# Kernel optimization log

Measured on AMD Instinct MI355X. Metric: run time of the kernel, lower is better.

## Reference

```python
import jax, jax.numpy as jnp
import numpy as np

K = 0.5   # k constant from init
QS = 0.1  # qs constant from init


def setup_inputs() -> dict:
    key = jax.random.key(0)
    k1, k2, k3 = jax.random.split(key, 3)
    B, OUT, M, IN = 512, 128, 8, 512
    x = jax.random.normal(k1, (B, IN), dtype=jnp.float32)
    W = jax.random.uniform(k2, (OUT, M, IN), dtype=jnp.float32)
    q = jax.random.uniform(k3, (OUT, M, IN), dtype=jnp.float32)
    return {"x": x, "W": W, "q": q}


def reference(x, W, q):
    # x: [B, IN]; W, q: [OUT, M, IN]
    # dendritic: relu(k * (x*W - q)), summed over input dim
    syn = jax.nn.relu(K * (x[:, None, None, :] * W - q))  # [B, OUT, M, IN]
    dend = jax.nn.relu(jnp.sum(syn, axis=3))              # [B, OUT, M]
    soma = jnp.sum(dend, axis=2)                          # [B, OUT]
    return jax.nn.relu(K * (soma - QS))
```

## Files before the change

kernel.cpp:

```cpp
#include <hip/hip_runtime.h>


#define OUTN 128
#define MM   8
#define INN  512

typedef float    f4 __attribute__((ext_vector_type(4)));
typedef float    f2 __attribute__((ext_vector_type(2)));
typedef _Float16 h2 __attribute__((ext_vector_type(2)));
typedef _Float16 h4 __attribute__((ext_vector_type(4)));
typedef _Float16 h8 __attribute__((ext_vector_type(8)));

#define XH_ELEMS 262144
#define WH_ELEMS 524288

__global__ __launch_bounds__(256) void cvt_kernel(
    const float* __restrict__ x, const float* __restrict__ W,
    const float* __restrict__ q, _Float16* __restrict__ h)
{
    const int j = blockIdx.x * 256 + threadIdx.x;
    f4 v;
    if (j < 65536)        v = ((const f4*)x)[j];
    else if (j < 196608)  v = ((const f4*)W)[j - 65536];
    else                  v = ((const f4*)q)[j - 196608];
    ((h4*)h)[j] = __builtin_convertvector(v, h4);
}

__global__ __launch_bounds__(256) void dnm_kernel(
    const _Float16* __restrict__ xh,
    const _Float16* __restrict__ Wh,
    const _Float16* __restrict__ qh,
    float* __restrict__ out)
{
    __shared__ _Float16 lds_w[MM * INN];
    __shared__ _Float16 lds_q[MM * INN];

    const int tid  = threadIdx.x;
    const int o    = blockIdx.x >> 4;
    const int bgrp = blockIdx.x & 15;
    const int wave = tid >> 6;
    const int lane = tid & 63;
    const int b0   = bgrp * 32 + wave * 8;
    const int i0   = lane * 8;

    {
        const f4* Wg = (const f4*)(Wh + (size_t)o * MM * INN);
        const f4* qg = (const f4*)(qh + (size_t)o * MM * INN);
        f4* lw = (f4*)lds_w;
        f4* lq = (f4*)lds_q;
        lw[tid]       = Wg[tid];
        lw[tid + 256] = Wg[tid + 256];
        lq[tid]       = qg[tid];
        lq[tid + 256] = qg[tid + 256];
    }

    h8 xv[8];
    #pragma unroll
    for (int b = 0; b < 8; ++b)
        xv[b] = *(const h8*)(xh + (size_t)(b0 + b) * INN + i0);

    __syncthreads();

    float acc[8];
    #pragma unroll
    for (int b = 0; b < 8; ++b) acc[b] = 0.0f;

    const h2 one = {(_Float16)1.0f, (_Float16)1.0f};

    #pragma unroll 2
    for (int m = 0; m < MM; ++m) {
        const h8 w8 = *(const h8*)(lds_w + m * INN + i0);
        const h8 q8 = *(const h8*)(lds_q + m * INN + i0);
        #pragma unroll
        for (int b = 0; b < 8; ++b) {
            #pragma unroll
            for (int p = 0; p < 4; ++p) {
                h2 xx = {xv[b][2 * p], xv[b][2 * p + 1]};
                h2 ww = {w8[2 * p], w8[2 * p + 1]};
                h2 qq = {q8[2 * p], q8[2 * p + 1]};
                h2 t = __builtin_elementwise_fma(xx, ww, -qq);
                t = __builtin_elementwise_max(t, (h2)(_Float16)0.0f);
#if __has_builtin(__builtin_amdgcn_fdot2)
                acc[b] = __builtin_amdgcn_fdot2(t, one, acc[b], false);
#else
                acc[b] += (float)t[0] + (float)t[1];
#endif
            }
        }
    }

    #pragma unroll
    for (int b = 0; b < 8; ++b) {
        float v = acc[b];
        v += __shfl_xor(v, 1, 64);
        v += __shfl_xor(v, 2, 64);
        v += __shfl_xor(v, 4, 64);
        v += __shfl_xor(v, 8, 64);
        v += __shfl_xor(v, 16, 64);
        v += __shfl_xor(v, 32, 64);
        if (lane == b) {
            float r = 0.25f * v - 0.05f;
            out[(size_t)(b0 + b) * OUTN + o] = fmaxf(r, 0.0f);
        }
    }
}

extern "C" void kernel_launch(void* const* d_in, const int* in_sizes, int n_in,
                              void* d_out, int out_size, void* d_ws, size_t ws_size,
                              hipStream_t stream) {
    const float* x = (const float*)d_in[0];
    const float* W = (const float*)d_in[1];
    const float* q = (const float*)d_in[2];
    float* out = (float*)d_out;
    _Float16* h = (_Float16*)d_ws;

    cvt_kernel<<<dim3(1280), dim3(256), 0, stream>>>(x, W, q, h);

    const _Float16* xh = h;
    const _Float16* Wh = h + XH_ELEMS;
    const _Float16* qh = h + XH_ELEMS + WH_ELEMS;
    dnm_kernel<<<dim3(OUTN * 16), dim3(256), 0, stream>>>(xh, Wh, qh, out);
}
```

Before: 79.22 us.

## Drop LDS staging; each wave computes 4 outputs x 8 batches streaming W/q from global

Removes the shared-memory staging of W and q, so there is no block-wide barrier. Each wave now handles 4 output neurons for 8 batch rows and streams W/q rows straight from global memory with a one-step register prefetch. The grid shrinks from 2048 to 512 blocks, and each surviving lane writes one vectorized float4 of outputs. In exchange each lane holds 32 accumulators, which raises register pressure, and there are fewer waves to hide global load latency.

```diff
diff --git a/kernel.cpp b/kernel.cpp
--- a/kernel.cpp
+++ b/kernel.cpp
@@ -6,7 +6,6 @@
 #define INN  512
 
 typedef float    f4 __attribute__((ext_vector_type(4)));
-typedef float    f2 __attribute__((ext_vector_type(2)));
 typedef _Float16 h2 __attribute__((ext_vector_type(2)));
 typedef _Float16 h4 __attribute__((ext_vector_type(4)));
 typedef _Float16 h8 __attribute__((ext_vector_type(8)));
@@ -32,76 +31,79 @@
     const _Float16* __restrict__ qh,
     float* __restrict__ out)
 {
-    __shared__ _Float16 lds_w[MM * INN];
-    __shared__ _Float16 lds_q[MM * INN];
-
     const int tid  = threadIdx.x;
-    const int o    = blockIdx.x >> 4;
-    const int bgrp = blockIdx.x & 15;
     const int wave = tid >> 6;
     const int lane = tid & 63;
-    const int b0   = bgrp * 32 + wave * 8;
+    const int flat = blockIdx.x * 4 + wave;
+    const int ogrp = flat & 31;
+    const int bgrp = flat >> 5;
+    const int o0   = ogrp * 4;
+    const int b0   = bgrp * 8;
     const int i0   = lane * 8;
-
-    {
-        const f4* Wg = (const f4*)(Wh + (size_t)o * MM * INN);
-        const f4* qg = (const f4*)(qh + (size_t)o * MM * INN);
-        f4* lw = (f4*)lds_w;
-        f4* lq = (f4*)lds_q;
-        lw[tid]       = Wg[tid];
-        lw[tid + 256] = Wg[tid + 256];
-        lq[tid]       = qg[tid];
-        lq[tid + 256] = qg[tid + 256];
-    }
 
     h8 xv[8];
     #pragma unroll
     for (int b = 0; b < 8; ++b)
         xv[b] = *(const h8*)(xh + (size_t)(b0 + b) * INN + i0);
 
-    __syncthreads();
-
-    float acc[8];
+    float acc[32];
     #pragma unroll
-    for (int b = 0; b < 8; ++b) acc[b] = 0.0f;
+    for (int j = 0; j < 32; ++j) acc[j] = 0.0f;
 
     const h2 one = {(_Float16)1.0f, (_Float16)1.0f};
+    const size_t row0 = ((size_t)o0 * MM) * INN + i0;
 
-    #pragma unroll 2
-    for (int m = 0; m < MM; ++m) {
-        const h8 w8 = *(const h8*)(lds_w + m * INN + i0);
-        const h8 q8 = *(const h8*)(lds_q + m * INN + i0);
+    h8 wc = *(const h8*)(Wh + row0);
+    h8 qc = *(const h8*)(qh + row0);
+    #pragma unroll 1
+    for (int om = 0; om < 32; ++om) {
+        h8 wn, qn;
+        if (om < 31) {
+            const size_t rn = row0 + (size_t)(om + 1) * INN;
+            wn = *(const h8*)(Wh + rn);
+            qn = *(const h8*)(qh + rn);
+        }
+        float* ao = acc + (om >> 3) * 8;
         #pragma unroll
         for (int b = 0; b < 8; ++b) {
             #pragma unroll
             for (int p = 0; p < 4; ++p) {
                 h2 xx = {xv[b][2 * p], xv[b][2 * p + 1]};
-                h2 ww = {w8[2 * p], w8[2 * p + 1]};
-                h2 qq = {q8[2 * p], q8[2 * p + 1]};
+                h2 ww = {wc[2 * p], wc[2 * p + 1]};
+                h2 qq = {qc[2 * p], qc[2 * p + 1]};
                 h2 t = __builtin_elementwise_fma(xx, ww, -qq);
                 t = __builtin_elementwise_max(t, (h2)(_Float16)0.0f);
 #if __has_builtin(__builtin_amdgcn_fdot2)
-                acc[b] = __builtin_amdgcn_fdot2(t, one, acc[b], false);
+                ao[b] = __builtin_amdgcn_fdot2(t, one, ao[b], false);
 #else
-                acc[b] += (float)t[0] + (float)t[1];
+                ao[b] += (float)t[0] + (float)t[1];
 #endif
             }
         }
+        wc = wn; qc = qn;
     }
 
     #pragma unroll
-    for (int b = 0; b < 8; ++b) {
-        float v = acc[b];
+    for (int j = 0; j < 32; ++j) {
+        float v = acc[j];
         v += __shfl_xor(v, 1, 64);
         v += __shfl_xor(v, 2, 64);
         v += __shfl_xor(v, 4, 64);
         v += __shfl_xor(v, 8, 64);
         v += __shfl_xor(v, 16, 64);
         v += __shfl_xor(v, 32, 64);
-        if (lane == b) {
-            float r = 0.25f * v - 0.05f;
-            out[(size_t)(b0 + b) * OUTN + o] = fmaxf(r, 0.0f);
+        acc[j] = v;
+    }
+
+    if (lane < 8) {
+        const int b = lane;
+        f4 r;
+        #pragma unroll
+        for (int ol = 0; ol < 4; ++ol) {
+            float v = 0.25f * acc[ol * 8 + b] - 0.05f;
+            r[ol] = fmaxf(v, 0.0f);
         }
+        *(f4*)(out + (size_t)(b0 + b) * OUTN + o0) = r;
     }
 }
 
@@ -119,5 +121,5 @@
     const _Float16* xh = h;
     const _Float16* Wh = h + XH_ELEMS;
     const _Float16* qh = h + XH_ELEMS + WH_ELEMS;
-    dnm_kernel<<<dim3(OUTN * 16), dim3(256), 0, stream>>>(xh, Wh, qh, out);
+    dnm_kernel<<<dim3(512), dim3(256), 0, stream>>>(xh, Wh, qh, out);
 }
```

Result: slower. 87.22 us (+10.1%).

## Process four batch tiles per block with register-cached W/q and prefetched x

Applied to the files above, without the earlier changes.

Each block now covers 128 batch rows instead of 32, so grid size drops from 2048 to 512 blocks. The W/q tile for the output neuron is loaded from LDS into registers once and reused across four passes, and the next pass's x rows are prefetched into registers during the current pass. This cuts redundant LDS staging of W/q per block and reduces per-block overhead. The cost is higher register pressure (wf/qf/xv/xn arrays) and fewer blocks, which may hurt occupancy and latency hiding on a GPU with many CUs.

```diff
diff --git a/kernel.cpp b/kernel.cpp
--- a/kernel.cpp
+++ b/kernel.cpp
@@ -6,7 +6,6 @@
 #define INN  512
 
 typedef float    f4 __attribute__((ext_vector_type(4)));
-typedef float    f2 __attribute__((ext_vector_type(2)));
 typedef _Float16 h2 __attribute__((ext_vector_type(2)));
 typedef _Float16 h4 __attribute__((ext_vector_type(4)));
 typedef _Float16 h8 __attribute__((ext_vector_type(8)));
@@ -36,12 +35,12 @@
     __shared__ _Float16 lds_q[MM * INN];
 
     const int tid  = threadIdx.x;
-    const int o    = blockIdx.x >> 4;
-    const int bgrp = blockIdx.x & 15;
+    const int o    = blockIdx.x >> 2;
+    const int bgrp = blockIdx.x & 3;
     const int wave = tid >> 6;
     const int lane = tid & 63;
-    const int b0   = bgrp * 32 + wave * 8;
     const int i0   = lane * 8;
+    const int bw   = bgrp * 128 + wave * 32;
 
     {
         const f4* Wg = (const f4*)(Wh + (size_t)o * MM * INN);
@@ -54,54 +53,72 @@
         lq[tid + 256] = qg[tid + 256];
     }
 
-    h8 xv[8];
+    h8 xv[8], xn[8];
     #pragma unroll
     for (int b = 0; b < 8; ++b)
-        xv[b] = *(const h8*)(xh + (size_t)(b0 + b) * INN + i0);
+        xv[b] = *(const h8*)(xh + (size_t)(bw + b) * INN + i0);
 
     __syncthreads();
 
-    float acc[8];
+    h8 wf[MM], qf[MM];
     #pragma unroll
-    for (int b = 0; b < 8; ++b) acc[b] = 0.0f;
+    for (int m = 0; m < MM; ++m) {
+        wf[m] = *(const h8*)(lds_w + m * INN + i0);
+        qf[m] = *(const h8*)(lds_q + m * INN + i0);
+    }
 
     const h2 one = {(_Float16)1.0f, (_Float16)1.0f};
 
-    #pragma unroll 2
-    for (int m = 0; m < MM; ++m) {
-        const h8 w8 = *(const h8*)(lds_w + m * INN + i0);
-        const h8 q8 = *(const h8*)(lds_q + m * INN + i0);
+    #pragma unroll 1
+    for (int pass = 0; pass < 4; ++pass) {
+        if (pass < 3) {
+            #pragma unroll
+            for (int b = 0; b < 8; ++b)
+                xn[b] = *(const h8*)(xh + (size_t)(bw + (pass + 1) * 8 + b) * INN + i0);
+        }
+
+        float acc[8];
+        #pragma unroll
+        for (int b = 0; b < 8; ++b) acc[b] = 0.0f;
+
+        #pragma unroll
+        for (int m = 0; m < MM; ++m) {
+            #pragma unroll
+            for (int b = 0; b < 8; ++b) {
+                #pragma unroll
+                for (int p = 0; p < 4; ++p) {
+                    h2 xx = {xv[b][2 * p], xv[b][2 * p + 1]};
+                    h2 ww = {wf[m][2 * p], wf[m][2 * p + 1]};
+                    h2 qq = {qf[m][2 * p], qf[m][2 * p + 1]};
+                    h2 t = __builtin_elementwise_fma(xx, ww, -qq);
+                    t = __builtin_elementwise_max(t, (h2)(_Float16)0.0f);
+#if __has_builtin(__builtin_amdgcn_fdot2)
+                    acc[b] = __builtin_amdgcn_fdot2(t, one, acc[b], false);
+#else
+                    acc[b] += (float)t[0] + (float)t[1];
+#endif
+                }
+            }
+        }
+
+        const int b0 = bw + pass * 8;
         #pragma unroll
         for (int b = 0; b < 8; ++b) {
-            #pragma unroll
-            for (int p = 0; p < 4; ++p) {
-                h2 xx = {xv[b][2 * p], xv[b][2 * p + 1]};
-                h2 ww = {w8[2 * p], w8[2 * p + 1]};
-                h2 qq = {q8[2 * p], q8[2 * p + 1]};
-                h2 t = __builtin_elementwise_fma(xx, ww, -qq);
-                t = __builtin_elementwise_max(t, (h2)(_Float16)0.0f);
-#if __has_builtin(__builtin_amdgcn_fdot2)
-                acc[b] = __builtin_amdgcn_fdot2(t, one, acc[b], false);
-#else
-                acc[b] += (float)t[0] + (float)t[1];
-#endif
+            float v = acc[b];
+            v += __shfl_xor(v, 1, 64);
+            v += __shfl_xor(v, 2, 64);
+            v += __shfl_xor(v, 4, 64);
+            v += __shfl_xor(v, 8, 64);
+            v += __shfl_xor(v, 16, 64);
+            v += __shfl_xor(v, 32, 64);
+            if (lane == b) {
+                float r = 0.25f * v - 0.05f;
+                out[(size_t)(b0 + b) * OUTN + o] = fmaxf(r, 0.0f);
             }
         }
-    }
 
-    #pragma unroll
-    for (int b = 0; b < 8; ++b) {
-        float v = acc[b];
-        v += __shfl_xor(v, 1, 64);
-        v += __shfl_xor(v, 2, 64);
-        v += __shfl_xor(v, 4, 64);
-        v += __shfl_xor(v, 8, 64);
-        v += __shfl_xor(v, 16, 64);
-        v += __shfl_xor(v, 32, 64);
-        if (lane == b) {
-            float r = 0.25f * v - 0.05f;
-            out[(size_t)(b0 + b) * OUTN + o] = fmaxf(r, 0.0f);
-        }
+        #pragma unroll
+        for (int b = 0; b < 8; ++b) xv[b] = xn[b];
     }
 }
 
@@ -119,5 +136,5 @@
     const _Float16* xh = h;
     const _Float16* Wh = h + XH_ELEMS;
     const _Float16* qh = h + XH_ELEMS + WH_ELEMS;
-    dnm_kernel<<<dim3(OUTN * 16), dim3(256), 0, stream>>>(xh, Wh, qh, out);
+    dnm_kernel<<<dim3(512), dim3(256), 0, stream>>>(xh, Wh, qh, out);
 }
```

Result: slower. 84.25 us (+6.3%).
